# Optimization experiments

Hardware: AMD Instinct MI355X
Metric: run time of the kernel (lower is better)

## Reference

```python
import jax, jax.numpy as jnp
import numpy as np

D_MODEL = 1024; D_INNER = 2048; HEADDIM = 64; NHEADS = 32; DSTATE = 128
NGROUPS = 1; DCONV = 4; CHUNK = 256; EPS = 1e-5
D_IN_PROJ = 2 * D_INNER + 2 * NGROUPS * DSTATE + NHEADS
CONV_DIM = D_INNER + 2 * NGROUPS * DSTATE
B_SZ = 2; L_SEQ = 4096


def segsum(x):
    # x: (..., T) -> (..., T, T) lower-triangular segment sums (off-diag = -inf)
    T = x.shape[-1]
    cs = jnp.cumsum(x, axis=-1)
    ss = cs[..., :, None] - cs[..., None, :]
    return jnp.where(jnp.tril(jnp.ones((T, T), bool)), ss, -jnp.inf)


def ssd(x, dt, A, Bm, Cm):
    # Chunked SSD selective scan (Mamba2). x:(b,l,h,p) dt:(b,l,h) A:(h,) Bm,Cm:(b,l,g,n)
    b, l, h, p = x.shape
    c = l // CHUNK
    x = x.reshape(b, c, CHUNK, h, p)
    dt = dt.reshape(b, c, CHUNK, h)
    rep = h // NGROUPS
    Bh = jnp.repeat(Bm.reshape(b, c, CHUNK, NGROUPS, DSTATE), rep, axis=3)
    Ch = jnp.repeat(Cm.reshape(b, c, CHUNK, NGROUPS, DSTATE), rep, axis=3)
    xdt = x * dt[..., None]                       # discretized input dt*x
    Adt = (dt * A).transpose(0, 3, 1, 2)          # (b,h,c,T)
    A_cs = jnp.cumsum(Adt, axis=-1)
    Lmat = jnp.exp(segsum(Adt))                   # (b,h,c,T,T) intra-chunk decays
    Y_diag = jnp.einsum('bcthn,bcshn,bhcts,bcshp->bcthp', Ch, Bh, Lmat, xdt)
    decay_states = jnp.exp(A_cs[..., -1:] - A_cs)  # (b,h,c,T)
    states = jnp.einsum('bcthn,bhct,bcthp->bchpn', Bh, decay_states, xdt)
    A_pad = jnp.pad(A_cs[..., -1], ((0, 0), (0, 0), (1, 0)))  # (b,h,c+1)
    decay_chunk = jnp.exp(segsum(A_pad))          # (b,h,c+1,c+1) inter-chunk recurrence
    states = jnp.concatenate([jnp.zeros_like(states[:, :1]), states], axis=1)
    prev = jnp.einsum('bhzc,bchpn->bzhpn', decay_chunk, states)[:, :-1]
    Y_off = jnp.einsum('bcthn,bchpn,bhct->bcthp', Ch, prev, jnp.exp(A_cs))
    return (Y_diag + Y_off).reshape(b, l, h, p)


def mamba_dir(zxbcdt, conv_w, conv_b, dt_bias, A_log, Dp, norm_w):
    # One direction of mamba_split_conv1d_scan_combined (silu act, gated RMSNorm).
    b, l, _ = zxbcdt.shape
    z = zxbcdt[..., :D_INNER]
    xBC = zxbcdt[..., D_INNER:D_INNER + CONV_DIM]
    dt_raw = zxbcdt[..., D_INNER + CONV_DIM:]
    # causal depthwise conv1d (kernel=DCONV) + silu
    xp = jnp.pad(xBC, ((0, 0), (DCONV - 1, 0), (0, 0)))
    conv = conv_b
    for k in range(DCONV):
        conv = conv + conv_w[:, k] * xp[:, k:k + l, :]
    xBC = jax.nn.silu(conv)
    x = xBC[..., :D_INNER].reshape(b, l, NHEADS, HEADDIM)
    Bm = xBC[..., D_INNER:D_INNER + NGROUPS * DSTATE].reshape(b, l, NGROUPS, DSTATE)
    Cm = xBC[..., D_INNER + NGROUPS * DSTATE:].reshape(b, l, NGROUPS, DSTATE)
    dt = jax.nn.softplus(dt_raw + dt_bias)        # (b,l,h)
    A = -jnp.exp(A_log.astype(jnp.float32))       # (h,)
    y = ssd(x, dt, A, Bm, Cm) + x * Dp[None, None, :, None]  # D skip on raw x
    y = y.reshape(b, l, D_INNER)
    y = y * jax.nn.silu(z)                        # gate BEFORE norm (norm_before_gate=False)
    y = y * jax.lax.rsqrt(jnp.mean(y * y, axis=-1, keepdims=True) + EPS) * norm_w
    return y


def setup_inputs():
    rng = np.random.default_rng(0)
    f32 = lambda a: jnp.asarray(a, jnp.float32)
    # dt_bias init per BiMamba2.__init__
    dt = np.exp(rng.uniform(size=NHEADS) * (np.log(0.1) - np.log(0.001)) + np.log(0.001))
    dt = np.clip(dt, 1e-4, None)
    inv_dt = dt + np.log(-np.expm1(-dt))
    A_log = np.log(rng.uniform(1.0, 16.0, NHEADS))
    return dict(
        u=f32(rng.standard_normal((B_SZ, L_SEQ, D_MODEL))),
        in_proj_w=f32(rng.standard_normal((D_IN_PROJ, D_MODEL)) * 0.02),
        conv_w=f32(rng.standard_normal((CONV_DIM, DCONV)) * 0.2),
        conv_b=f32(np.zeros(CONV_DIM)),
        dt_bias=f32(inv_dt),
        A_log=f32(A_log),
        D=f32(np.ones(NHEADS)),
        norm_w=f32(np.ones(D_INNER)),
        bi_conv_w=f32(rng.standard_normal((CONV_DIM, DCONV)) * 0.2),
        bi_conv_b=f32(np.zeros(CONV_DIM)),
        bi_dt_bias=f32(inv_dt.copy()),
        bi_A_log=f32(A_log.copy()),
        bi_D=f32(np.ones(NHEADS)),
        bi_norm_w=f32(np.ones(D_INNER)),
        out_proj_w=f32(rng.standard_normal((D_MODEL, D_INNER)) * 0.02),
    )


def reference(u, in_proj_w, conv_w, conv_b, dt_bias, A_log, D, norm_w,
              bi_conv_w, bi_conv_b, bi_dt_bias, bi_A_log, bi_D, bi_norm_w, out_proj_w):
    zxbcdt = jnp.einsum('bld,ed->ble', u, in_proj_w)
    fwd = mamba_dir(zxbcdt, conv_w, conv_b, dt_bias, A_log, D, norm_w)
    bwd = mamba_dir(zxbcdt[:, ::-1], bi_conv_w, bi_conv_b, bi_dt_bias, bi_A_log, bi_D, bi_norm_w)
    out = (fwd + bwd[:, ::-1]) * 0.5
    return jnp.einsum('ble,de->bld', out, out_proj_w)
```

## Files before the change

### kernel.cpp

```cpp
#include <hip/hip_runtime.h>

#define LSEQ 4096
#define BSZ 2
#define DMODEL 1024
#define DINNER 2048
#define NHEADS 32
#define HEADDIM 64
#define DSTATE 128
#define CHUNK 256
#define NCHUNK 16
#define CONVDIM 2304
#define DINPROJ 4384
#define NPAD 4480
#define BL (BSZ*LSEQ)

typedef unsigned short u16;
typedef unsigned int u32;
typedef u16 u16x4 __attribute__((ext_vector_type(4)));
typedef u16 u16x8 __attribute__((ext_vector_type(8)));
typedef __bf16 bf16x8 __attribute__((ext_vector_type(8)));
typedef float f32x4 __attribute__((ext_vector_type(4)));

__device__ __forceinline__ u16 f2bf(float f){
  union { float f; u32 u; } v; v.f = f;
  u32 r = v.u + 0x7fffu + ((v.u >> 16) & 1u);
  return (u16)(r >> 16);
}
__device__ __forceinline__ float bf2f(u16 h){
  union { u32 u; float f; } v; v.u = ((u32)h) << 16;
  return v.f;
}
__device__ __forceinline__ u32 pack2(float a, float b){
  return (u32)f2bf(a) | ((u32)f2bf(b) << 16);
}
__device__ __forceinline__ f32x4 mfma16(bf16x8 a, bf16x8 b, f32x4 c){
  return __builtin_amdgcn_mfma_f32_16x16x32_bf16(a, b, c, 0, 0, 0);
}
__device__ __forceinline__ void gload16(const void* g, void* l){
  __builtin_amdgcn_global_load_lds((const __attribute__((address_space(1))) void*)g,
                                   (__attribute__((address_space(3))) void*)l, 16, 0, 0);
}

__global__ void sentinel_kernel(float* out){ out[threadIdx.x] = 123456.0f; }

__global__ void cvt_kernel(const float* __restrict__ in, u16* __restrict__ out,
                           long nin, long nout){
  long i = (long)blockIdx.x*blockDim.x + threadIdx.x;
  long stride = (long)gridDim.x*blockDim.x;
  for (; i < nout; i += stride) out[i] = (i < nin) ? f2bf(in[i]) : (u16)0;
}

template<int BF16OUT>
__global__ __launch_bounds__(256) void gemm_bt(const u16* __restrict__ A, const u16* __restrict__ B,
                                               void* __restrict__ Cv, int K, int ldc)
{
  __shared__ u16 As[4096];
  __shared__ u16 Bs[4096];
  const int tid = threadIdx.x, lane = tid & 63;
  const int wave = tid >> 6;
  const int wr = wave >> 1, wc = wave & 1;
  f32x4 acc[4][4];
  #pragma unroll
  for (int i=0;i<4;i++)
    #pragma unroll
    for (int j=0;j<4;j++) acc[i][j] = (f32x4){0.f,0.f,0.f,0.f};

  const u16* Ag = A + (size_t)blockIdx.x * 128 * K;
  const u16* Bg = B + (size_t)blockIdx.y * 128 * K;
  const u16* srcG = ((wave < 2) ? Ag : Bg) + (size_t)((wave & 1) * 64) * K;
  u16* dstL = ((wave < 2) ? As : Bs) + (wave & 1) * 64 * 32;
  const int lrow = lane >> 2;
  const int scol = ((lane & 3) ^ ((lane >> 3) & 3));
  const int r = lane & 15, g = lane >> 4;
  const int sg = (g ^ ((r >> 1) & 3)) * 8;

  for (int kt = 0; kt < K; kt += 32) {
    __syncthreads();
    #pragma unroll
    for (int i=0;i<4;i++){
      const u16* gp = srcG + (size_t)(i*16 + lrow)*K + kt + scol*8;
      gload16(gp, dstL + i*512);
    }
    __syncthreads();
    bf16x8 af[4], bfv[4];
    #pragma unroll
    for (int mt=0;mt<4;mt++) af[mt] = *(const bf16x8*)&As[(wr*64+mt*16+r)*32 + sg];
    #pragma unroll
    for (int nt=0;nt<4;nt++) bfv[nt] = *(const bf16x8*)&Bs[(wc*64+nt*16+r)*32 + sg];
    #pragma unroll
    for (int mt=0;mt<4;mt++)
      #pragma unroll
      for (int nt=0;nt<4;nt++)
        acc[mt][nt] = mfma16(af[mt], bfv[nt], acc[mt][nt]);
  }
  const size_t cbase = (size_t)(blockIdx.x*128 + wr*64 + g*4) * ldc
                     + blockIdx.y*128 + wc*64 + r;
  if (BF16OUT) {
    u16* Cg = (u16*)Cv + cbase;
    #pragma unroll
    for (int mt=0;mt<4;mt++)
      #pragma unroll
      for (int nt=0;nt<4;nt++)
        #pragma unroll
        for (int j=0;j<4;j++)
          Cg[(size_t)(mt*16+j)*ldc + nt*16] = f2bf(acc[mt][nt][j]);
  } else {
    float* Cg = (float*)Cv + cbase;
    #pragma unroll
    for (int mt=0;mt<4;mt++)
      #pragma unroll
      for (int nt=0;nt<4;nt++)
        #pragma unroll
        for (int j=0;j<4;j++)
          Cg[(size_t)(mt*16+j)*ldc + nt*16] = acc[mt][nt][j];
  }
}

__global__ __launch_bounds__(320) void conv_kernel(
    const u16* __restrict__ zxh, const float* __restrict__ cw, const float* __restrict__ cb,
    const float* __restrict__ dtb,
    u16* __restrict__ xout, u16* __restrict__ Bout, u16* __restrict__ Cout,
    float* __restrict__ dtt, int rev)
{
  const int l = blockIdx.x, b = blockIdx.y, tid = threadIdx.x;
  if (tid < 288){
    const int ch0 = tid*8;
    f32x4 cw4[8];
    #pragma unroll
    for (int j=0;j<8;j++) cw4[j] = *(const f32x4*)&cw[(ch0+j)*4];
    float acc[8];
    {
      f32x4 b0 = *(const f32x4*)&cb[ch0];
      f32x4 b1 = *(const f32x4*)&cb[ch0+4];
      #pragma unroll
      for (int j=0;j<4;j++){ acc[j] = b0[j]; acc[4+j] = b1[j]; }
    }
    #pragma unroll
    for (int k=0;k<4;k++){
      int ls = l - 3 + k;
      if (ls >= 0){
        int lsrc = rev ? (LSEQ-1-ls) : ls;
        u16x8 v = *(const u16x8*)(zxh + ((size_t)b*LSEQ + lsrc)*NPAD + DINNER + ch0);
        #pragma unroll
        for (int j=0;j<8;j++) acc[j] += cw4[j][k] * bf2f(v[j]);
      }
    }
    u16x8 o;
    #pragma unroll
    for (int j=0;j<8;j++){
      float sv = acc[j] / (1.f + __expf(-acc[j]));
      o[j] = f2bf(sv);
    }
    if (ch0 < DINNER)
      *(u16x8*)(xout + ((size_t)b*LSEQ + l)*DINNER + ch0) = o;
    else if (ch0 < DINNER+DSTATE)
      *(u16x8*)(Bout + ((size_t)b*LSEQ + l)*DSTATE + (ch0 - DINNER)) = o;
    else
      *(u16x8*)(Cout + ((size_t)b*LSEQ + l)*DSTATE + (ch0 - DINNER - DSTATE)) = o;
  } else {
    const int hh = tid - 288;
    const int lsrc = rev ? (LSEQ-1-l) : l;
    float raw = bf2f(zxh[((size_t)b*LSEQ + lsrc)*NPAD + DINNER + CONVDIM + hh]) + dtb[hh];
    float dv = (raw > 20.f) ? raw : log1pf(__expf(raw));
    dtt[((size_t)b*NHEADS + hh)*LSEQ + l] = dv;
  }
}

__global__ __launch_bounds__(256) void acs_kernel(const float* __restrict__ dtt,
    const float* __restrict__ A_log, float* __restrict__ acs)
{
  const int c = blockIdx.x, hh = blockIdx.y, b = blockIdx.z;
  const int t = threadIdx.x;
  __shared__ float s[CHUNK];
  const float Ah = -__expf(A_log[hh]);
  const size_t base = ((size_t)b*NHEADS + hh)*LSEQ + (size_t)c*CHUNK;
  s[t] = dtt[base + t] * Ah;
  __syncthreads();
  for (int off=1; off<CHUNK; off<<=1){
    float add = (t >= off) ? s[t-off] : 0.f;
    __syncthreads();
    s[t] += add;
    __syncthreads();
  }
  acs[base + t] = s[t];
}

__global__ __launch_bounds__(256) void states_kernel(
    const u16* __restrict__ xb, const u16* __restrict__ Bb,
    const float* __restrict__ dtt, const float* __restrict__ acs,
    u16* __restrict__ states)
{
  const int h = blockIdx.x, c = blockIdx.y, b = blockIdx.z;
  const int tid = threadIdx.x, lane = tid & 63, w = tid >> 6;
  __shared__ float acs_s[CHUNK], dt_s[CHUNK];
  __shared__ u32 xdtTW[64*20];
  __shared__ u32 BsdW[128*20];

  const size_t bhBase = ((size_t)b*NHEADS + h)*LSEQ + (size_t)c*CHUNK;
  acs_s[tid] = acs[bhBase + tid];
  dt_s[tid]  = dtt[bhBase + tid];
  __syncthreads();
  const float acsLast = acs_s[CHUNK-1];

  f32x4 sacc[4][2];
  #pragma unroll
  for (int i=0;i<4;i++){ sacc[i][0] = (f32x4){0,0,0,0}; sacc[i][1] = (f32x4){0,0,0,0}; }

  const int s2 = tid >> 4, q = tid & 15;
  const int g = lane >> 4, r = lane & 15;
  const size_t rowBase = (size_t)b*LSEQ + (size_t)c*CHUNK;
  for (int st8 = 0; st8 < 8; ++st8) {
    const int s0 = st8*32;
    const int sA = s0 + 2*s2, sB = sA + 1;
    u16x4 xA = *(const u16x4*)(xb + (rowBase+sA)*DINNER + h*HEADDIM + 4*q);
    u16x4 xB4 = *(const u16x4*)(xb + (rowBase+sB)*DINNER + h*HEADDIM + 4*q);
    u16x8 bA = *(const u16x8*)(Bb + (rowBase+sA)*DSTATE + 8*q);
    u16x8 bB = *(const u16x8*)(Bb + (rowBase+sB)*DSTATE + 8*q);
    const float dA = dt_s[sA], dB = dt_s[sB];
    const float eA = __expf(acsLast - acs_s[sA]), eB = __expf(acsLast - acs_s[sB]);
    __syncthreads();
    #pragma unroll
    for (int j=0;j<4;j++){
      int p = 4*q + j;
      xdtTW[p*20 + (s2 ^ (((p>>3)&3)<<2))] = pack2(bf2f(xA[j])*dA, bf2f(xB4[j])*dB);
    }
    #pragma unroll
    for (int j=0;j<8;j++){
      int n = 8*q + j;
      BsdW[n*20 + (s2 ^ (((n>>3)&3)<<2))] = pack2(bf2f(bA[j])*eA, bf2f(bB[j])*eB);
    }
    __syncthreads();
    bf16x8 xf[4];
    #pragma unroll
    for (int pt=0;pt<4;pt++){
      int p = pt*16 + r;
      xf[pt] = *(const bf16x8*)&xdtTW[p*20 + 4*(g ^ ((p>>3)&3))];
    }
    #pragma unroll
    for (int nt=0;nt<2;nt++){
      int n = w*32 + nt*16 + r;
      bf16x8 bdf = *(const bf16x8*)&BsdW[n*20 + 4*(g ^ ((n>>3)&3))];
      #pragma unroll
      for (int pt=0;pt<4;pt++) sacc[pt][nt] = mfma16(xf[pt], bdf, sacc[pt][nt]);
    }
  }
  u16* sp = states + (((size_t)b*NCHUNK + c)*NHEADS + h)*(size_t)(HEADDIM*DSTATE);
  #pragma unroll
  for (int pt=0;pt<4;pt++)
    #pragma unroll
    for (int nt=0;nt<2;nt++)
      #pragma unroll
      for (int j=0;j<4;j++)
        sp[(size_t)(pt*16+g*4+j)*DSTATE + w*32+nt*16+r] = f2bf(sacc[pt][nt][j]);
}

__global__ __launch_bounds__(256) void recur_kernel(const u16* __restrict__ states,
    const float* __restrict__ acs, u16* __restrict__ prev)
{
  const int b = blockIdx.x >> 5, h = blockIdx.x & 31;
  const int tid = threadIdx.x;
  float S[32];
  #pragma unroll
  for (int k=0;k<32;k++) S[k] = 0.f;
  for (int c=0;c<NCHUNK;c++){
    const size_t off = (((size_t)b*NCHUNK + c)*NHEADS + h)*(size_t)(HEADDIM*DSTATE);
    const float dc = __expf(acs[((size_t)b*NHEADS+h)*LSEQ + (size_t)c*CHUNK + CHUNK-1]);
    #pragma unroll
    for (int k=0;k<32;k++){
      const size_t i = off + tid + k*256;
      prev[i] = f2bf(S[k]);
      S[k] = S[k]*dc + bf2f(states[i]);
    }
  }
}

__global__ __launch_bounds__(256) void ydiagoff_kernel(
    const u16* __restrict__ xb, const u16* __restrict__ Bb, const u16* __restrict__ Cb,
    const float* __restrict__ dtt, const float* __restrict__ acs,
    const u16* __restrict__ prev, const float* __restrict__ Dp,
    u16* __restrict__ ydir)
{
  const int h = blockIdx.x, c = blockIdx.y, b = blockIdx.z;
  const int tid = threadIdx.x, lane = tid & 63, w = tid >> 6;
  __shared__ float acs_s[CHUNK], dt_s[CHUNK];
  __shared__ u16 Bs[32][136];
  __shared__ u32 xdtTW[64*20];
  __shared__ u16 Ms[4][64][40];

  const size_t bhBase = ((size_t)b*NHEADS + h)*LSEQ + (size_t)c*CHUNK;
  acs_s[tid] = acs[bhBase + tid];
  dt_s[tid]  = dtt[bhBase + tid];
  __syncthreads();

  const int g = lane >> 4, r = lane & 15;
  const size_t rowBase = (size_t)b*LSEQ + (size_t)c*CHUNK;

  bf16x8 caf[4][4];
  const u16* Crow = Cb + rowBase*DSTATE;
  #pragma unroll
  for (int mt=0;mt<4;mt++)
    #pragma unroll
    for (int ks=0;ks<4;ks++)
      caf[mt][ks] = *(const bf16x8*)(Crow + (size_t)(w*64+mt*16+r)*DSTATE + ks*32 + g*8);

  f32x4 yacc[4][4];
  #pragma unroll
  for (int i=0;i<4;i++)
    #pragma unroll
    for (int j=0;j<4;j++) yacc[i][j] = (f32x4){0,0,0,0};

  const int sl = tid >> 3, part = tid & 7;
  const int s2 = tid >> 4, q = tid & 15;
  for (int st8 = 0; st8 < 8; ++st8) {
    const int s0 = st8*32;
    u16x8 v0 = *(const u16x8*)(Bb + (rowBase + s0 + sl)*DSTATE + part*16);
    u16x8 v1 = *(const u16x8*)(Bb + (rowBase + s0 + sl)*DSTATE + part*16 + 8);
    const int sA = s0 + 2*s2, sB = sA + 1;
    u16x4 xA = *(const u16x4*)(xb + (rowBase+sA)*DINNER + h*HEADDIM + 4*q);
    u16x4 xB4 = *(const u16x4*)(xb + (rowBase+sB)*DINNER + h*HEADDIM + 4*q);
    const float dA = dt_s[sA], dB = dt_s[sB];
    __syncthreads();
    *(u16x8*)&Bs[sl][part*16]   = v0;
    *(u16x8*)&Bs[sl][part*16+8] = v1;
    #pragma unroll
    for (int j=0;j<4;j++){
      int p = 4*q + j;
      xdtTW[p*20 + (s2 ^ (((p>>3)&3)<<2))] = pack2(bf2f(xA[j])*dA, bf2f(xB4[j])*dB);
    }
    __syncthreads();
    f32x4 g2[4][2];
    #pragma unroll
    for (int i=0;i<4;i++){ g2[i][0] = (f32x4){0,0,0,0}; g2[i][1] = (f32x4){0,0,0,0}; }
    #pragma unroll
    for (int ks=0;ks<4;ks++){
      bf16x8 bfv0 = *(const bf16x8*)&Bs[r][ks*32+g*8];
      bf16x8 bfv1 = *(const bf16x8*)&Bs[16+r][ks*32+g*8];
      #pragma unroll
      for (int mt=0;mt<4;mt++){
        g2[mt][0] = mfma16(caf[mt][ks], bfv0, g2[mt][0]);
        g2[mt][1] = mfma16(caf[mt][ks], bfv1, g2[mt][1]);
      }
    }
    #pragma unroll
    for (int mt=0;mt<4;mt++)
      #pragma unroll
      for (int st=0;st<2;st++)
        #pragma unroll
        for (int j=0;j<4;j++){
          int tl = w*64 + mt*16 + g*4 + j;
          int sg2 = s0 + st*16 + r;
          float v = (sg2 <= tl) ? g2[mt][st][j]*__expf(acs_s[tl]-acs_s[sg2]) : 0.f;
          Ms[w][mt*16+g*4+j][st*16+r] = f2bf(v);
        }
    bf16x8 xf[4];
    #pragma unroll
    for (int pt=0;pt<4;pt++){
      int p = pt*16 + r;
      xf[pt] = *(const bf16x8*)&xdtTW[p*20 + 4*(g ^ ((p>>3)&3))];
    }
    #pragma unroll
    for (int mt=0;mt<4;mt++){
      bf16x8 mf = *(const bf16x8*)&Ms[w][mt*16+r][g*8];
      #pragma unroll
      for (int pt=0;pt<4;pt++) yacc[mt][pt] = mfma16(mf, xf[pt], yacc[mt][pt]);
    }
  }
  #pragma unroll
  for (int mt=0;mt<4;mt++){
    const float et = __expf(acs_s[w*64 + mt*16 + r]);
    #pragma unroll
    for (int ks=0;ks<4;ks++)
      #pragma unroll
      for (int e=0;e<8;e++)
        caf[mt][ks][e] = (__bf16)((float)caf[mt][ks][e] * et);
  }
  const u16* pv = prev + (((size_t)b*NCHUNK + c)*NHEADS + h)*(size_t)(HEADDIM*DSTATE);
  #pragma unroll
  for (int ks=0;ks<4;ks++){
    bf16x8 pf[4];
    #pragma unroll
    for (int pt=0;pt<4;pt++)
      pf[pt] = *(const bf16x8*)(pv + (size_t)(pt*16+r)*DSTATE + ks*32 + g*8);
    #pragma unroll
    for (int mt=0;mt<4;mt++)
      #pragma unroll
      for (int pt=0;pt<4;pt++) yacc[mt][pt] = mfma16(caf[mt][ks], pf[pt], yacc[mt][pt]);
  }
  const float Dh = Dp[h];
  const u16* xrow = xb + rowBase*DINNER + h*HEADDIM;
  u16* yrow = ydir + rowBase*DINNER + h*HEADDIM;
  #pragma unroll
  for (int mt=0;mt<4;mt++)
    #pragma unroll
    for (int pt=0;pt<4;pt++)
      #pragma unroll
      for (int j=0;j<4;j++){
        int tl = w*64 + mt*16 + g*4 + j;
        int p  = pt*16 + r;
        float xv = bf2f(xrow[(size_t)tl*DINNER + p]);
        yrow[(size_t)tl*DINNER + p] = f2bf(yacc[mt][pt][j] + xv*Dh);
      }
}

__global__ __launch_bounds__(256) void gate_norm_kernel(
    const u16* __restrict__ ydir, const u16* __restrict__ zxh,
    const float* __restrict__ nw, u16* __restrict__ ybufh, int rev)
{
  const int l = blockIdx.x, b = blockIdx.y, tid = threadIdx.x;
  const int lsrc = rev ? (LSEQ-1-l) : l;
  u16x8 zv = *(const u16x8*)(zxh + ((size_t)b*LSEQ + lsrc)*NPAD + tid*8);
  u16x8 yv = *(const u16x8*)(ydir + ((size_t)b*LSEQ + l)*DINNER + tid*8);
  float gg[8]; float ss = 0.f;
  #pragma unroll
  for (int j=0;j<8;j++){
    float z = bf2f(zv[j]);
    float y = bf2f(yv[j]);
    float v = y * (z / (1.f + __expf(-z)));
    gg[j] = v; ss += v*v;
  }
  #pragma unroll
  for (int off=32; off>0; off>>=1) ss += __shfl_xor(ss, off, 64);
  __shared__ float red[4];
  if ((tid&63)==0) red[tid>>6] = ss;
  __syncthreads();
  float tot = red[0]+red[1]+red[2]+red[3];
  float scale = rsqrtf(tot * (1.f/DINNER) + 1e-5f);
  const float* nwp = nw + tid*8;
  u16* hrow = ybufh + ((size_t)b*LSEQ + lsrc)*DINNER + tid*8;
  u16x8 o;
  if (!rev){
    #pragma unroll
    for (int j=0;j<8;j++) o[j] = f2bf(0.5f * gg[j]*scale*nwp[j]);
  } else {
    u16x8 pvv = *(const u16x8*)hrow;
    #pragma unroll
    for (int j=0;j<8;j++) o[j] = f2bf(bf2f(pvv[j]) + 0.5f*gg[j]*scale*nwp[j]);
  }
  *(u16x8*)hrow = o;
}

extern "C" void kernel_launch(void* const* d_in, const int* in_sizes, int n_in,
                              void* d_out, int out_size, void* d_ws, size_t ws_size,
                              hipStream_t stream) {
  const float* u        = (const float*)d_in[0];
  const float* w1       = (const float*)d_in[1];
  const float* conv_w   = (const float*)d_in[2];
  const float* conv_b   = (const float*)d_in[3];
  const float* dt_bias  = (const float*)d_in[4];
  const float* A_log    = (const float*)d_in[5];
  const float* Dp       = (const float*)d_in[6];
  const float* norm_w   = (const float*)d_in[7];
  const float* bconv_w  = (const float*)d_in[8];
  const float* bconv_b  = (const float*)d_in[9];
  const float* bdt_bias = (const float*)d_in[10];
  const float* bA_log   = (const float*)d_in[11];
  const float* bDp      = (const float*)d_in[12];
  const float* bnorm_w  = (const float*)d_in[13];
  const float* wo       = (const float*)d_in[14];
  float* out = (float*)d_out;

  const size_t SZ_ZX  = (size_t)BL*NPAD*2;
  const size_t SZ_UB  = (size_t)BL*DMODEL*2;
  const size_t SZ_W1  = (size_t)NPAD*DMODEL*2;
  const size_t SZ_WO  = (size_t)DMODEL*DINNER*2;
  const size_t SZ_XB  = (size_t)BL*DINNER*2;
  const size_t SZ_BB  = (size_t)BL*DSTATE*2;
  const size_t SZ_DT  = (size_t)BSZ*NHEADS*LSEQ*4;
  const size_t SZ_ST  = (size_t)BSZ*NCHUNK*NHEADS*HEADDIM*DSTATE*2;
  const size_t SZ_YD  = (size_t)BL*DINNER*2;
  const size_t SZ_YH  = (size_t)BL*DINNER*2;
  const size_t NEED = SZ_ZX + SZ_UB + SZ_W1 + SZ_WO + SZ_XB + 2*SZ_BB + 2*SZ_DT
                    + SZ_ST + SZ_YD + SZ_YH;
  if (ws_size < NEED) { sentinel_kernel<<<1,256,0,stream>>>(out); return; }

  char* p = (char*)d_ws;
  u16*   zxh    = (u16*)p;              p += SZ_ZX;
  u16*   ub     = (u16*)p;              p += SZ_UB;
  u16*   states = ub;
  u16*   w1b    = (u16*)p;              p += SZ_W1;
  u16*   wob    = (u16*)p;              p += SZ_WO;
  u16*   xb     = (u16*)p;              p += SZ_XB;
  u16*   Bb     = (u16*)p;              p += SZ_BB;
  u16*   Cb     = (u16*)p;              p += SZ_BB;
  float* dtt    = (float*)p;            p += SZ_DT;
  float* acs    = (float*)p;            p += SZ_DT;
  u16*   prev   = (u16*)p;              p += SZ_ST;
  u16*   ydir   = (u16*)p;              p += SZ_YD;
  u16*   ybufh  = (u16*)p;              p += SZ_YH;

  cvt_kernel<<<2048,256,0,stream>>>(u,  ub,  (long)BL*DMODEL,      (long)BL*DMODEL);
  cvt_kernel<<<2048,256,0,stream>>>(w1, w1b, (long)DINPROJ*DMODEL, (long)NPAD*DMODEL);
  cvt_kernel<<<2048,256,0,stream>>>(wo, wob, (long)DMODEL*DINNER,  (long)DMODEL*DINNER);

  gemm_bt<1><<<dim3(BL/128, NPAD/128),256,0,stream>>>(ub, w1b, zxh, DMODEL, NPAD);

  for (int dir = 0; dir < 2; ++dir) {
    const float* cwp = dir ? bconv_w  : conv_w;
    const float* cbp = dir ? bconv_b  : conv_b;
    const float* dbp = dir ? bdt_bias : dt_bias;
    const float* alp = dir ? bA_log   : A_log;
    const float* ddp = dir ? bDp      : Dp;
    const float* nwp = dir ? bnorm_w  : norm_w;
    conv_kernel<<<dim3(LSEQ,BSZ),320,0,stream>>>(zxh, cwp, cbp, dbp, xb, Bb, Cb, dtt, dir);
    acs_kernel<<<dim3(NCHUNK,NHEADS,BSZ),256,0,stream>>>(dtt, alp, acs);
    states_kernel<<<dim3(NHEADS,NCHUNK,BSZ),256,0,stream>>>(xb, Bb, dtt, acs, states);
    recur_kernel<<<BSZ*NHEADS,256,0,stream>>>(states, acs, prev);
    ydiagoff_kernel<<<dim3(NHEADS,NCHUNK,BSZ),256,0,stream>>>(xb, Bb, Cb, dtt, acs, prev, ddp, ydir);
    gate_norm_kernel<<<dim3(LSEQ,BSZ),256,0,stream>>>(ydir, zxh, nwp, ybufh, dir);
  }

  gemm_bt<0><<<dim3(BL/128, DMODEL/128),256,0,stream>>>(ybufh, wob, out, DINNER, DMODEL);
}
```

Before: 539.4 us.

## Interleave row tiles across warps and skip fully masked causal tiles in SSD chunk kernel

Rows of each chunk are now assigned to warps in an interleaved way (mt*64 + w*16) instead of contiguous 64-row blocks. Each warp's load then stays balanced when work is cut. For each 32-column source tile, the C·B^T MFMAs, the decay masking and the M·xdt MFMAs are skipped when the 16-row tile lies entirely above the causal diagonal. This removes about half of the intra-chunk matmul work. The cost is divergent branching per row tile and a loop body the compiler may schedule less well.

```diff
diff --git a/kernel.cpp b/kernel.cpp
--- a/kernel.cpp
+++ b/kernel.cpp
@@ -301,7 +301,7 @@
   for (int mt=0;mt<4;mt++)
     #pragma unroll
     for (int ks=0;ks<4;ks++)
-      caf[mt][ks] = *(const bf16x8*)(Crow + (size_t)(w*64+mt*16+r)*DSTATE + ks*32 + g*8);
+      caf[mt][ks] = *(const bf16x8*)(Crow + (size_t)(mt*64+w*16+r)*DSTATE + ks*32 + g*8);
 
   f32x4 yacc[4][4];
   #pragma unroll
@@ -328,30 +328,6 @@
       xdtTW[p*20 + (s2 ^ (((p>>3)&3)<<2))] = pack2(bf2f(xA[j])*dA, bf2f(xB4[j])*dB);
     }
     __syncthreads();
-    f32x4 g2[4][2];
-    #pragma unroll
-    for (int i=0;i<4;i++){ g2[i][0] = (f32x4){0,0,0,0}; g2[i][1] = (f32x4){0,0,0,0}; }
-    #pragma unroll
-    for (int ks=0;ks<4;ks++){
-      bf16x8 bfv0 = *(const bf16x8*)&Bs[r][ks*32+g*8];
-      bf16x8 bfv1 = *(const bf16x8*)&Bs[16+r][ks*32+g*8];
-      #pragma unroll
-      for (int mt=0;mt<4;mt++){
-        g2[mt][0] = mfma16(caf[mt][ks], bfv0, g2[mt][0]);
-        g2[mt][1] = mfma16(caf[mt][ks], bfv1, g2[mt][1]);
-      }
-    }
-    #pragma unroll
-    for (int mt=0;mt<4;mt++)
-      #pragma unroll
-      for (int st=0;st<2;st++)
-        #pragma unroll
-        for (int j=0;j<4;j++){
-          int tl = w*64 + mt*16 + g*4 + j;
-          int sg2 = s0 + st*16 + r;
-          float v = (sg2 <= tl) ? g2[mt][st][j]*__expf(acs_s[tl]-acs_s[sg2]) : 0.f;
-          Ms[w][mt*16+g*4+j][st*16+r] = f2bf(v);
-        }
     bf16x8 xf[4];
     #pragma unroll
     for (int pt=0;pt<4;pt++){
@@ -360,14 +336,34 @@
     }
     #pragma unroll
     for (int mt=0;mt<4;mt++){
-      bf16x8 mf = *(const bf16x8*)&Ms[w][mt*16+r][g*8];
-      #pragma unroll
-      for (int pt=0;pt<4;pt++) yacc[mt][pt] = mfma16(mf, xf[pt], yacc[mt][pt]);
+      if (4*mt + w >= 2*st8) {
+        f32x4 g20 = (f32x4){0,0,0,0}, g21 = (f32x4){0,0,0,0};
+        #pragma unroll
+        for (int ks=0;ks<4;ks++){
+          bf16x8 bfv0 = *(const bf16x8*)&Bs[r][ks*32+g*8];
+          bf16x8 bfv1 = *(const bf16x8*)&Bs[16+r][ks*32+g*8];
+          g20 = mfma16(caf[mt][ks], bfv0, g20);
+          g21 = mfma16(caf[mt][ks], bfv1, g21);
+        }
+        #pragma unroll
+        for (int j=0;j<4;j++){
+          int tl = mt*64 + w*16 + g*4 + j;
+          int sg0 = s0 + r;
+          int sg1 = s0 + 16 + r;
+          float m0 = (sg0 <= tl) ? g20[j]*__expf(acs_s[tl]-acs_s[sg0]) : 0.f;
+          float m1 = (sg1 <= tl) ? g21[j]*__expf(acs_s[tl]-acs_s[sg1]) : 0.f;
+          Ms[w][mt*16+g*4+j][r]    = f2bf(m0);
+          Ms[w][mt*16+g*4+j][16+r] = f2bf(m1);
+        }
+        bf16x8 mf = *(const bf16x8*)&Ms[w][mt*16+r][g*8];
+        #pragma unroll
+        for (int pt=0;pt<4;pt++) yacc[mt][pt] = mfma16(mf, xf[pt], yacc[mt][pt]);
+      }
     }
   }
   #pragma unroll
   for (int mt=0;mt<4;mt++){
-    const float et = __expf(acs_s[w*64 + mt*16 + r]);
+    const float et = __expf(acs_s[mt*64 + w*16 + r]);
     #pragma unroll
     for (int ks=0;ks<4;ks++)
       #pragma unroll
@@ -395,7 +391,7 @@
     for (int pt=0;pt<4;pt++)
       #pragma unroll
       for (int j=0;j<4;j++){
-        int tl = w*64 + mt*16 + g*4 + j;
+        int tl = mt*64 + w*16 + g*4 + j;
         int p  = pt*16 + r;
         float xv = bf2f(xrow[(size_t)tl*DINNER + p]);
         yrow[(size_t)tl*DINNER + p] = f2bf(yacc[mt][pt][j] + xv*Dh);
```

Result: faster. 518.1 us (-4.0%).
